# Performance work log

Measured on AMD Instinct MI355X. Metric: run time of the kernel, lower is better.

Reference implementation:

```python
import jax, jax.numpy as jnp
import numpy as np

N, D, V, S = 65536, 768, 32000, 8192
LN_EPS = 1e-5


def setup_inputs() -> dict:
    key = jax.random.key(0)
    ks = jax.random.split(key, 5)
    # Build targets with exactly S runs of equal consecutive ids (words).
    rng = np.random.default_rng(0)
    cuts = np.sort(rng.choice(np.arange(1, N), size=S - 1, replace=False))
    bounds = np.concatenate([np.array([0]), cuts, np.array([N])])
    lens = np.diff(bounds)  # S run lengths, each >= 1, sum == N
    seg_vals = np.arange(S) % V  # adjacent segment ids always differ
    targets = np.repeat(seg_vals, lens).astype(np.int64)
    inv_sqrt_d = 1.0 / np.sqrt(D).astype(np.float32)
    return {
        "features": jax.random.normal(ks[0], (N, D), jnp.float32),
        "targets_sp": jnp.asarray(targets),
        "num_words": S,
        "W_dense": jax.random.normal(ks[1], (D, D), jnp.float32) * inv_sqrt_d,
        "b_dense": jnp.zeros((D,), jnp.float32),
        "ln_gamma": jnp.ones((D,), jnp.float32),
        "ln_beta": jnp.zeros((D,), jnp.float32),
        "W_vocab": jax.random.normal(ks[2], (V, D), jnp.float32) * inv_sqrt_d,
        "b_vocab": jnp.zeros((V,), jnp.float32),
    }


def _layer_norm(x, gamma, beta):
    mu = jnp.mean(x, axis=-1, keepdims=True)
    var = jnp.mean(jnp.square(x - mu), axis=-1, keepdims=True)
    return (x - mu) * jax.lax.rsqrt(var + LN_EPS) * gamma + beta


def reference(features, targets_sp, num_words, W_dense, b_dense, ln_gamma, ln_beta, W_vocab, b_vocab):
    # word begins where target differs from previous token (first token always begins)
    prev = jnp.concatenate([jnp.array([-1], dtype=targets_sp.dtype), targets_sp[:-1]])
    new_word = prev != targets_sp  # True at segment starts
    seg_id = jnp.cumsum(new_word.astype(jnp.int32)) - 1  # [N], values in [0, num_words)

    # per-segment mean pool (single segment-reduce pass instead of python loop)
    sums = jax.ops.segment_sum(features, seg_id, num_segments=num_words)  # [S, D]
    counts = jax.ops.segment_sum(jnp.ones((features.shape[0],), features.dtype), seg_id, num_segments=num_words)
    pooled = sums / counts[:, None]

    # per-segment target (all tokens in a run share the same id)
    seg_targets = jax.ops.segment_max(targets_sp, seg_id, num_segments=num_words)

    x = pooled @ W_dense.T + b_dense
    x = jax.nn.gelu(x, approximate=False)
    x = _layer_norm(x, ln_gamma, ln_beta)
    logits = x @ W_vocab.T + b_vocab  # [S, V]
    return (logits, seg_targets)
```

## Files before the change

### kernel.cpp

```cpp
#include <hip/hip_runtime.h>
#include <hip/hip_bf16.h>
#include <cstdint>

#define NTOK 65536
#define DDIM 768
#define VOC  32000
#define SEG  8192

typedef unsigned short ushort_t;
typedef __attribute__((ext_vector_type(8))) __bf16 bf16x8;
typedef __attribute__((ext_vector_type(4))) float  f32x4;

__device__ __forceinline__ ushort_t f2bf(float f) {
  uint32_t u = __builtin_bit_cast(uint32_t, f);
  return (ushort_t)((u + 0x7fffu + ((u >> 16) & 1u)) >> 16);
}

__global__ __launch_bounds__(256) void cvt_bf16(const float4* __restrict__ in,
                                                ushort4* __restrict__ out, int n4) {
  int i = blockIdx.x * 256 + threadIdx.x;
  if (i >= n4) return;
  float4 v = in[i];
  ushort4 o;
  o.x = f2bf(v.x); o.y = f2bf(v.y); o.z = f2bf(v.z); o.w = f2bf(v.w);
  out[i] = o;
}

__global__ __launch_bounds__(256) void seg_count(const int* __restrict__ t,
                                                 int* __restrict__ blockCnt) {
  int i = blockIdx.x * 256 + threadIdx.x;
  bool flag = (i == 0) || (t[i] != t[i - 1]);
  unsigned long long b = __ballot(flag);
  __shared__ int wsum[4];
  int lane = threadIdx.x & 63, w = threadIdx.x >> 6;
  if (lane == 0) wsum[w] = __popcll(b);
  __syncthreads();
  if (threadIdx.x == 0)
    blockCnt[blockIdx.x] = wsum[0] + wsum[1] + wsum[2] + wsum[3];
}

__global__ void seg_scan(const int* __restrict__ blockCnt, int* __restrict__ blockOff,
                         int* __restrict__ starts) {
  if (threadIdx.x == 0) {
    int acc = 0;
    for (int b = 0; b < NTOK / 256; ++b) { blockOff[b] = acc; acc += blockCnt[b]; }
    starts[SEG] = NTOK;
  }
}

__global__ __launch_bounds__(256) void seg_emit(const int* __restrict__ t,
                                                const int* __restrict__ blockOff,
                                                int* __restrict__ starts,
                                                float* __restrict__ segt_out) {
  int i = blockIdx.x * 256 + threadIdx.x;
  bool flag = (i == 0) || (t[i] != t[i - 1]);
  unsigned long long b = __ballot(flag);
  int lane = threadIdx.x & 63, w = threadIdx.x >> 6;
  __shared__ int woff[4];
  if (lane == 0) woff[w] = __popcll(b);
  __syncthreads();
  if (threadIdx.x == 0) {
    int a = 0;
    for (int j = 0; j < 4; ++j) { int c = woff[j]; woff[j] = a; a += c; }
  }
  __syncthreads();
  if (flag) {
    int rank = blockOff[blockIdx.x] + woff[w] +
               __popcll(b & ((1ull << lane) - 1ull));
    starts[rank] = i;
    segt_out[rank] = (float)t[i];
  }
}

__global__ __launch_bounds__(256) void pool_k(const float* __restrict__ feat,
                                              const int* __restrict__ starts,
                                              ushort_t* __restrict__ pooled) {
  int s = blockIdx.x;
  int rs = starts[s], re = starts[s + 1];
  float inv = 1.0f / (float)(re - rs);
  int tid = threadIdx.x;
  float a0 = 0.f, a1 = 0.f, a2 = 0.f;
  for (int r = rs; r < re; ++r) {
    const float* row = feat + (size_t)r * DDIM;
    a0 += row[tid]; a1 += row[tid + 256]; a2 += row[tid + 512];
  }
  size_t base = (size_t)s * DDIM;
  pooled[base + tid]       = f2bf(a0 * inv);
  pooled[base + tid + 256] = f2bf(a1 * inv);
  pooled[base + tid + 512] = f2bf(a2 * inv);
}

__global__ __launch_bounds__(256) void ln_k(const float* __restrict__ X,
                                            const float* __restrict__ gamma,
                                            const float* __restrict__ beta,
                                            ushort_t* __restrict__ Y) {
  int row = blockIdx.x;
  const float* x = X + (size_t)row * DDIM;
  int tid = threadIdx.x;
  float v0 = x[tid], v1 = x[tid + 256], v2 = x[tid + 512];
  __shared__ float sh[4];
  int lane = tid & 63, w = tid >> 6;

  float s = v0 + v1 + v2;
#pragma unroll
  for (int o = 32; o > 0; o >>= 1) s += __shfl_xor(s, o, 64);
  if (lane == 0) sh[w] = s;
  __syncthreads();
  float mu = (sh[0] + sh[1] + sh[2] + sh[3]) * (1.0f / DDIM);
  __syncthreads();

  float d0 = v0 - mu, d1 = v1 - mu, d2 = v2 - mu;
  float q = d0 * d0 + d1 * d1 + d2 * d2;
#pragma unroll
  for (int o = 32; o > 0; o >>= 1) q += __shfl_xor(q, o, 64);
  if (lane == 0) sh[w] = q;
  __syncthreads();
  float var = (sh[0] + sh[1] + sh[2] + sh[3]) * (1.0f / DDIM);
  float inv = rsqrtf(var + 1e-5f);

  size_t base = (size_t)row * DDIM;
  Y[base + tid]       = f2bf(d0 * inv * gamma[tid] + beta[tid]);
  Y[base + tid + 256] = f2bf(d1 * inv * gamma[tid + 256] + beta[tid + 256]);
  Y[base + tid + 512] = f2bf(d2 * inv * gamma[tid + 512] + beta[tid + 512]);
}


#define DO_MFMA(mh, nh)                                                        \
  __builtin_amdgcn_s_setprio(1);                                               \
  _Pragma("unroll")                                                            \
  for (int kk = 0; kk < 2; ++kk)                                               \
    _Pragma("unroll")                                                          \
    for (int f2 = 0; f2 < 4; ++f2)                                             \
      _Pragma("unroll")                                                        \
      for (int g2 = 0; g2 < 2; ++g2)                                           \
        acc[(mh)*4 + f2][(nh)*2 + g2] = __builtin_amdgcn_mfma_f32_16x16x32_bf16( \
            aF[f2][kk], bF[nh][g2][kk], acc[(mh)*4 + f2][(nh)*2 + g2], 0, 0, 0); \
  __builtin_amdgcn_s_setprio(0);

#define LOAD_A(mh)                                                             \
  _Pragma("unroll")                                                            \
  for (int f2 = 0; f2 < 4; ++f2)                                               \
    _Pragma("unroll")                                                          \
    for (int kk = 0; kk < 2; ++kk)                                             \
      aF[f2][kk] = *(const bf16x8*)(tb + (((aByte + (mh)*8192 + f2*2048)) ^ (kk << 6)));

#define LOAD_B(nh)                                                             \
  _Pragma("unroll")                                                            \
  for (int g2 = 0; g2 < 2; ++g2)                                               \
    _Pragma("unroll")                                                          \
    for (int kk = 0; kk < 2; ++kk)                                             \
      bF[nh][g2][kk] = *(const bf16x8*)(tb + (((bByte + (nh)*4096 + g2*2048)) ^ (kk << 6)));

#define STAGE_HT(tt, h, gptr)                                                  \
  do {                                                                         \
    char* hb = lds + (((tt) & 1) * 65536) + (h) * 16384 + w * 2048;            \
    const ushort_t* gp = (gptr) + (size_t)(tt) * 64;                           \
    __builtin_amdgcn_global_load_lds(                                          \
        (const __attribute__((address_space(1))) void*)(gp),                   \
        (__attribute__((address_space(3))) void*)(hb), 16, 0, 0);              \
    __builtin_amdgcn_global_load_lds(                                          \
        (const __attribute__((address_space(1))) void*)(gp + rowK8),           \
        (__attribute__((address_space(3))) void*)(hb + 1024), 16, 0, 0);       \
  } while (0)

#define WAITV(n)  asm volatile("s_waitcnt vmcnt(" #n ")" ::: "memory")
#define WAITL     asm volatile("s_waitcnt lgkmcnt(0)" ::: "memory")
#define BAR       __builtin_amdgcn_s_barrier()

template <bool GELU>
__global__ __launch_bounds__(512, 2) void gemm256(const ushort_t* __restrict__ A,
                                                  const ushort_t* __restrict__ B,
                                                  const float* __restrict__ bias,
                                                  float* __restrict__ C,
                                                  int M, int Nn, int K) {
  __shared__ __align__(16) char lds[131072];
  const int tid = threadIdx.x, w = tid >> 6, lane = tid & 63;
  const int NT = K >> 6;

  const int nbx = Nn >> 8, nby = M >> 8, nwg = nbx * nby;
  const int bid = (int)blockIdx.x;
  const int swzb = (bid & 7) * (nwg >> 3) + (bid >> 3);
  const int by = swzb / nbx, bx = swzb - by * nbx;
  const int m0 = by << 8, n0 = bx << 8;

  const int srow = w * 16 + (lane >> 3);
  const int scol = ((lane & 7) ^ (lane >> 3)) << 3;
  const ushort_t* gA = A + (size_t)(m0 + srow) * K + scol;
  const ushort_t* gB = B + (size_t)(n0 + srow) * K + scol;
  const size_t rowK8 = (size_t)8 * K, rowK128 = (size_t)128 * K;

  const int fr_ = lane & 15, c16 = lane >> 4;
  const int xorv = (fr_ & 7) << 4;
  const int aByte = ((w >> 2) << 14) + (fr_ << 7) + ((c16 << 4) ^ xorv);
  const int bByte = 32768 + (((w & 3) >> 1) << 14) +
                    ((((w & 1) << 6) + fr_) << 7) + ((c16 << 4) ^ xorv);

  f32x4 acc[8][4] = {};
  bf16x8 aF[4][2], bF[2][2][2];

  STAGE_HT(0, 0, gA);
  STAGE_HT(0, 2, gB);
  STAGE_HT(0, 3, gB + rowK128);
  STAGE_HT(0, 1, gA + rowK128);
  STAGE_HT(1, 0, gA);
  STAGE_HT(1, 2, gB);
  STAGE_HT(1, 3, gB + rowK128);
  WAITV(6);
  BAR;

  for (int t = 0; t < NT - 2; ++t) {
    const char* tb = lds + (t & 1) * 65536;

    STAGE_HT(t + 1, 1, gA + rowK128);
    LOAD_A(0); LOAD_B(0);
    BAR; WAITL;
    DO_MFMA(0, 0);
    WAITV(10); BAR;

    STAGE_HT(t + 2, 0, gA);
    LOAD_B(1);
    BAR; WAITL;
    DO_MFMA(0, 1);
    WAITV(10); BAR;

    STAGE_HT(t + 2, 2, gB);
    LOAD_A(1);
    BAR; WAITL;
    DO_MFMA(1, 1);
    BAR;

    STAGE_HT(t + 2, 3, gB + rowK128);
    DO_MFMA(1, 0);
    WAITV(10); BAR;
  }

  {
    const int t = NT - 2;
    const char* tb = lds + (t & 1) * 65536;
    STAGE_HT(t + 1, 1, gA + rowK128);
    LOAD_A(0); LOAD_B(0);
    BAR; WAITL;
    DO_MFMA(0, 0);
    WAITV(10); BAR;

    LOAD_B(1);
    BAR; WAITL;
    DO_MFMA(0, 1);
    WAITV(8); BAR;

    LOAD_A(1);
    BAR; WAITL;
    DO_MFMA(1, 1);
    BAR;

    DO_MFMA(1, 0);
    WAITV(4); BAR;
  }

  {
    const int t = NT - 1;
    const char* tb = lds + (t & 1) * 65536;
    LOAD_A(0); LOAD_B(0);
    BAR; WAITL;
    DO_MFMA(0, 0);
    WAITV(2); BAR;

    LOAD_B(1);
    BAR; WAITL;
    DO_MFMA(0, 1);
    WAITV(0); BAR;

    LOAD_A(1);
    BAR; WAITL;
    DO_MFMA(1, 1);
    BAR;

    DO_MFMA(1, 0);
  }

  const int wr = (w >> 2) << 7, wc = (w & 3) << 6;
  const int crow = (lane >> 4) << 2, ccol = lane & 15;
#pragma unroll
  for (int g = 0; g < 4; ++g) {
    const int gcol = n0 + wc + g * 16 + ccol;
    const float bvv = bias[gcol];
#pragma unroll
    for (int f = 0; f < 8; ++f) {
      const int grow = m0 + wr + f * 16 + crow;
#pragma unroll
      for (int r = 0; r < 4; ++r) {
        float v = acc[f][g][r] + bvv;
        if (GELU) v = 0.5f * v * (1.0f + erff(v * 0.70710678118654752f));
        C[(size_t)(grow + r) * Nn + gcol] = v;
      }
    }
  }
}

extern "C" void kernel_launch(void* const* d_in, const int* in_sizes, int n_in,
                              void* d_out, int out_size, void* d_ws, size_t ws_size,
                              hipStream_t stream) {
  const float* features = (const float*)d_in[0];
  const int*   targets  = (const int*)d_in[1];
  const float* Wd    = (const float*)d_in[3];
  const float* bd    = (const float*)d_in[4];
  const float* gamma = (const float*)d_in[5];
  const float* beta  = (const float*)d_in[6];
  const float* Wv    = (const float*)d_in[7];
  const float* bv    = (const float*)d_in[8];
  float* out = (float*)d_out;

  ushort_t* wv_bf  = (ushort_t*)d_ws;
  ushort_t* wd_bf  = wv_bf + (size_t)VOC * DDIM;
  ushort_t* pooled = wd_bf + (size_t)DDIM * DDIM;
  ushort_t* xln    = pooled + (size_t)SEG * DDIM;
  float*    dense  = (float*)(xln + (size_t)SEG * DDIM);
  int*      starts = (int*)(dense + (size_t)SEG * DDIM);
  int*      blockCnt = starts + SEG + 4;
  int*      blockOff = blockCnt + NTOK / 256;

  cvt_bf16<<<(VOC * DDIM / 4 + 255) / 256, 256, 0, stream>>>(
      (const float4*)Wv, (ushort4*)wv_bf, VOC * DDIM / 4);
  cvt_bf16<<<(DDIM * DDIM / 4 + 255) / 256, 256, 0, stream>>>(
      (const float4*)Wd, (ushort4*)wd_bf, DDIM * DDIM / 4);

  seg_count<<<NTOK / 256, 256, 0, stream>>>(targets, blockCnt);
  seg_scan<<<1, 64, 0, stream>>>(blockCnt, blockOff, starts);
  seg_emit<<<NTOK / 256, 256, 0, stream>>>(targets, blockOff, starts,
                                           out + (size_t)SEG * VOC);

  pool_k<<<SEG, 256, 0, stream>>>(features, starts, pooled);

  gemm256<true><<<(SEG / 256) * (DDIM / 256), 512, 0, stream>>>(
      pooled, wd_bf, bd, dense, SEG, DDIM, DDIM);

  ln_k<<<SEG, 256, 0, stream>>>(dense, gamma, beta, xln);

  gemm256<false><<<(SEG / 256) * (VOC / 256), 512, 0, stream>>>(
      xln, wv_bf, bv, out, SEG, VOC, DDIM);
}
```

Before: 775.9 us.

## Restructure GEMM prefetch to stage full tiles two ahead with one wait per iteration

The GEMM main loop's global-to-LDS staging schedule changes. The prologue now stages two full K-tiles. Each iteration issues the t+2 tile's A and B quarter-loads in the second half and waits on vmcnt once at the end, instead of interleaving per-quarter waits after each MFMA phase. The separate tail iterations fold into a single loop with a guard, reducing mid-iteration synchronization stalls but keeping more loads in flight and risking LDS hazards if the buffer reuse timing is wrong.

```diff
diff --git a/kernel.cpp b/kernel.cpp
--- a/kernel.cpp
+++ b/kernel.cpp
@@ -198,84 +198,46 @@
   f32x4 acc[8][4] = {};
   bf16x8 aF[4][2], bF[2][2][2];
 
-  STAGE_HT(0, 0, gA);
   STAGE_HT(0, 2, gB);
   STAGE_HT(0, 3, gB + rowK128);
+  STAGE_HT(0, 0, gA);
   STAGE_HT(0, 1, gA + rowK128);
-  STAGE_HT(1, 0, gA);
   STAGE_HT(1, 2, gB);
   STAGE_HT(1, 3, gB + rowK128);
-  WAITV(6);
+  STAGE_HT(1, 0, gA);
+  STAGE_HT(1, 1, gA + rowK128);
+  WAITV(8);
   BAR;
 
-  for (int t = 0; t < NT - 2; ++t) {
+  for (int t = 0; t < NT; ++t) {
     const char* tb = lds + (t & 1) * 65536;
-
-    STAGE_HT(t + 1, 1, gA + rowK128);
+    const bool st = (t + 2 < NT);
+
     LOAD_A(0); LOAD_B(0);
     BAR; WAITL;
     DO_MFMA(0, 0);
-    WAITV(10); BAR;
-
-    STAGE_HT(t + 2, 0, gA);
+    BAR;
+
     LOAD_B(1);
     BAR; WAITL;
     DO_MFMA(0, 1);
-    WAITV(10); BAR;
-
-    STAGE_HT(t + 2, 2, gB);
+    BAR;
+
+    if (st) STAGE_HT(t + 2, 2, gB);
     LOAD_A(1);
     BAR; WAITL;
     DO_MFMA(1, 1);
     BAR;
 
-    STAGE_HT(t + 2, 3, gB + rowK128);
+    if (st) {
+      STAGE_HT(t + 2, 3, gB + rowK128);
+      STAGE_HT(t + 2, 0, gA);
+      STAGE_HT(t + 2, 1, gA + rowK128);
+    }
     DO_MFMA(1, 0);
-    WAITV(10); BAR;
-  }
-
-  {
-    const int t = NT - 2;
-    const char* tb = lds + (t & 1) * 65536;
-    STAGE_HT(t + 1, 1, gA + rowK128);
-    LOAD_A(0); LOAD_B(0);
-    BAR; WAITL;
-    DO_MFMA(0, 0);
-    WAITV(10); BAR;
-
-    LOAD_B(1);
-    BAR; WAITL;
-    DO_MFMA(0, 1);
-    WAITV(8); BAR;
-
-    LOAD_A(1);
-    BAR; WAITL;
-    DO_MFMA(1, 1);
+    if (st)                { WAITV(8); }
+    else if (t + 2 == NT)  { WAITV(0); }
     BAR;
-
-    DO_MFMA(1, 0);
-    WAITV(4); BAR;
-  }
-
-  {
-    const int t = NT - 1;
-    const char* tb = lds + (t & 1) * 65536;
-    LOAD_A(0); LOAD_B(0);
-    BAR; WAITL;
-    DO_MFMA(0, 0);
-    WAITV(2); BAR;
-
-    LOAD_B(1);
-    BAR; WAITL;
-    DO_MFMA(0, 1);
-    WAITV(0); BAR;
-
-    LOAD_A(1);
-    BAR; WAITL;
-    DO_MFMA(1, 1);
-    BAR;
-
-    DO_MFMA(1, 0);
   }
 
   const int wr = (w >> 2) << 7, wc = (w & 3) << 6;
```

Result: slower. 816.5 us (+5.2%).
